# Kernel tuning notes

Hardware: AMD Instinct MI355X
Metric: run time of the kernel (lower is better)

Reference implementation:

```python
import jax, jax.numpy as jnp
import numpy as np

NUM_HEADS = 8


def _layernorm(x, w, b, eps=1e-5):
    # normalize over last axis (channels)
    mu = jnp.mean(x, axis=-1, keepdims=True)
    var = jnp.var(x, axis=-1, keepdims=True)
    return (x - mu) * jax.lax.rsqrt(var + eps) * w + b


def setup_inputs() -> dict:
    key = jax.random.key(0)
    ks = jax.random.split(key, 5)
    B, C, H, W = 8, 512, 32, 32
    x = jax.random.normal(ks[0], (B, C, H, W), dtype=jnp.float32)
    ln_w = jnp.ones((C,), dtype=jnp.float32)
    ln_b = jnp.zeros((C,), dtype=jnp.float32)
    qkv_w = jax.random.normal(ks[1], (3 * C, C), dtype=jnp.float32) * (1.0 / np.sqrt(C))
    qkv_b = jax.random.normal(ks[2], (3 * C,), dtype=jnp.float32) * 0.02
    proj_w = jax.random.normal(ks[3], (C, C), dtype=jnp.float32) * (1.0 / np.sqrt(C))
    proj_b = jax.random.normal(ks[4], (C,), dtype=jnp.float32) * 0.02
    return {"x": x, "ln_w": ln_w, "ln_b": ln_b, "qkv_w": qkv_w,
            "qkv_b": qkv_b, "proj_w": proj_w, "proj_b": proj_b}


def reference(x, ln_w, ln_b, qkv_w, qkv_b, proj_w, proj_b):
    B, C, H, W = x.shape
    nh = NUM_HEADS
    hd = C // nh
    HW = H * W
    residual = x
    # LayerNorm over channels: (B,C,H,W) -> (B,H,W,C)
    xn = _layernorm(x.transpose(0, 2, 3, 1), ln_w, ln_b)  # (B,H,W,C)
    # 1x1 conv == per-pixel linear: (B,H,W,3C)
    qkv = jnp.einsum('bhwc,oc->bhwo', xn, qkv_w) + qkv_b
    # match torch reshape (B,3,nh,hd,HW).permute(1,0,2,4,3)
    qkv = qkv.reshape(B, HW, 3, nh, hd).transpose(2, 0, 3, 1, 4)  # (3,B,nh,HW,hd)
    q, k, v = qkv[0], qkv[1], qkv[2]
    scale = 1.0 / jnp.sqrt(jnp.asarray(hd, dtype=x.dtype))
    attn = jnp.einsum('bnqd,bnkd->bnqk', q, k) * scale  # (B,nh,HW,HW)
    attn = jax.nn.softmax(attn, axis=-1)
    out = jnp.einsum('bnqk,bnkd->bnqd', attn, v)  # (B,nh,HW,hd)
    out = out.transpose(0, 2, 1, 3).reshape(B, H, W, C)
    out = jnp.einsum('bhwc,oc->bhwo', out, proj_w) + proj_b
    return out.transpose(0, 3, 1, 2) + residual
```

## Files before the change

kernel.cpp:

```cpp
#include <hip/hip_runtime.h>

typedef __bf16 bf16;
typedef __bf16 bf16x8 __attribute__((ext_vector_type(8)));
typedef float f32x4 __attribute__((ext_vector_type(4)));
typedef float f32x16 __attribute__((ext_vector_type(16)));

#define MFMA16(a, b, c) __builtin_amdgcn_mfma_f32_16x16x32_bf16(a, b, c, 0, 0, 0)
#define MFMA32(a, b, c) __builtin_amdgcn_mfma_f32_32x32x16_bf16(a, b, c, 0, 0, 0)

#define QSCALE 0.1803368801111137f

static __device__ __forceinline__ unsigned int pack2(float a, float b) {
  unsigned short s0 = __builtin_bit_cast(unsigned short, (bf16)a);
  unsigned short s1 = __builtin_bit_cast(unsigned short, (bf16)b);
  return (unsigned int)s0 | ((unsigned int)s1 << 16);
}

static __device__ __forceinline__ void gl16(const bf16* g, bf16* l) {
  __builtin_amdgcn_global_load_lds(
      (const __attribute__((address_space(1))) unsigned int*)g,
      (__attribute__((address_space(3))) unsigned int*)l, 16, 0, 0);
}

__global__ __launch_bounds__(256) void convert_w(const float* __restrict__ qkvw,
                                                 const float* __restrict__ projw,
                                                 bf16* __restrict__ wc) {
  int c4 = blockIdx.x * 256 + threadIdx.x;
  const float* src = (c4 < 196608) ? (qkvw + (size_t)c4 * 4)
                                   : (projw + (size_t)(c4 - 196608) * 4);
  float4 v = *(const float4*)src;
  uint2 o;
  o.x = pack2(v.x, v.y);
  o.y = pack2(v.z, v.w);
  *(uint2*)&wc[(size_t)c4 * 4] = o;
}

__global__ __launch_bounds__(256) void ln_kernel(const float* __restrict__ x,
                                                 const float* __restrict__ lnw,
                                                 const float* __restrict__ lnb,
                                                 bf16* __restrict__ xn) {
  __shared__ float tile[512 * 17];
  __shared__ float wsh[512];
  __shared__ float bsh[512];
  const int t = threadIdx.x;
  const int b = blockIdx.x >> 6;
  const int p0 = (blockIdx.x & 63) * 16;
  for (int i = t; i < 512; i += 256) {
    wsh[i] = lnw[i];
    bsh[i] = lnb[i];
  }
  const float* xb = x + (size_t)b * 524288 + p0;
#pragma unroll
  for (int i = 0; i < 8; ++i) {
    int chunk = t + 256 * i;
    int c = chunk >> 2, px4 = (chunk & 3) * 4;
    float4 v = *(const float4*)&xb[(size_t)c * 1024 + px4];
    tile[c * 17 + px4 + 0] = v.x;
    tile[c * 17 + px4 + 1] = v.y;
    tile[c * 17 + px4 + 2] = v.z;
    tile[c * 17 + px4 + 3] = v.w;
  }
  __syncthreads();
  const int pix = t >> 4, j = t & 15;
  float sum = 0.f, sq = 0.f;
#pragma unroll
  for (int i = 0; i < 32; ++i) {
    int c = i * 16 + j;
    float v = tile[c * 17 + pix];
    sum += v;
    sq += v * v;
  }
#pragma unroll
  for (int m = 1; m <= 8; m <<= 1) {
    sum += __shfl_xor(sum, m);
    sq += __shfl_xor(sq, m);
  }
  float mu = sum * (1.f / 512.f);
  float var = sq * (1.f / 512.f) - mu * mu;
  float rstd = rsqrtf(var + 1e-5f);
  unsigned int* orow =
      (unsigned int*)(xn + ((size_t)(b * 1024 + p0 + pix)) * 512);
#pragma unroll
  for (int i = 0; i < 16; ++i) {
    int dw = i * 16 + j;
    int c0 = 2 * dw, c1 = 2 * dw + 1;
    float v0 = (tile[c0 * 17 + pix] - mu) * rstd * wsh[c0] + bsh[c0];
    float v1 = (tile[c1 * 17 + pix] - mu) * rstd * wsh[c1] + bsh[c1];
    orow[dw] = pack2(v0, v1);
  }
}

__global__ __launch_bounds__(256, 3) void gemm_qkv(
    const bf16* __restrict__ A, const bf16* __restrict__ Bm,
    const float* __restrict__ bias, bf16* __restrict__ oq,
    bf16* __restrict__ okk, bf16* __restrict__ ov) {
  __shared__ bf16 smem[16384];
  bf16* ash = smem;
  bf16* bsh = smem + 8192;
  const int t = threadIdx.x;
  const int lane = t & 63, w = t >> 6;
  const int quad = lane >> 4, r16 = lane & 15;
  const int wm = w >> 1, wn = w & 1;
  const int pid = blockIdx.x;
  const int panel = pid / 96, within = pid % 96;
  const int m0 = (panel * 8 + (within & 7)) * 128;
  const int n0 = (within >> 3) * 128;
  int soff[4];
  int sr[4];
#pragma unroll
  for (int j = 0; j < 4; ++j) {
    int c = (w * 4 + j) * 64 + lane;
    int r = c >> 3, cc = c & 7;
    sr[j] = r;
    soff[j] = (cc ^ (r & 7)) * 8;
  }
  f32x4 acc[4][4] = {};
  for (int k0 = 0; k0 < 512; k0 += 64) {
#pragma unroll
    for (int j = 0; j < 4; ++j) {
      gl16(&A[(size_t)(m0 + sr[j]) * 512 + k0 + soff[j]],
           &ash[(w * 4 + j) * 512]);
      gl16(&Bm[(size_t)(n0 + sr[j]) * 512 + k0 + soff[j]],
           &bsh[(w * 4 + j) * 512]);
    }
    __syncthreads();
#pragma unroll
    for (int kc = 0; kc < 2; ++kc) {
      bf16x8 af[4], bfr[4];
#pragma unroll
      for (int i = 0; i < 4; ++i) {
        int row = wm * 64 + i * 16 + r16;
        af[i] = *(const bf16x8*)&ash[row * 64 +
                                     ((kc * 4 + quad) ^ (r16 & 7)) * 8];
      }
#pragma unroll
      for (int i = 0; i < 4; ++i) {
        int row = wn * 64 + i * 16 + r16;
        bfr[i] = *(const bf16x8*)&bsh[row * 64 +
                                      ((kc * 4 + quad) ^ (r16 & 7)) * 8];
      }
#pragma unroll
      for (int tm = 0; tm < 4; ++tm)
#pragma unroll
        for (int tn = 0; tn < 4; ++tn)
          acc[tm][tn] = MFMA16(af[tm], bfr[tn], acc[tm][tn]);
    }
    __syncthreads();
  }
  if (n0 < 1024) {
#pragma unroll
    for (int tm = 0; tm < 4; ++tm) {
#pragma unroll
      for (int tn = 0; tn < 4; ++tn) {
        int n = n0 + wn * 64 + tn * 16 + r16;
        float bn = bias[n];
        int comp = n >> 9, h = (n >> 6) & 7, d = n & 63;
#pragma unroll
        for (int r = 0; r < 4; ++r) {
          int m = m0 + wm * 64 + tm * 16 + quad * 4 + r;
          float v = acc[tm][tn][r] + bn;
          int b = m >> 10, p = m & 1023;
          size_t base = ((size_t)(b * 8 + h)) * 65536;
          if (comp == 0)
            oq[base + (size_t)p * 64 + d] = (bf16)(v * QSCALE);
          else
            okk[base + (size_t)p * 64 + d] = (bf16)v;
        }
      }
    }
  } else {
    bf16* tb = &smem[w * 4096];
#pragma unroll
    for (int tn = 0; tn < 4; ++tn) {
      int n = n0 + wn * 64 + tn * 16 + r16;
      float bn = bias[n];
      int row = tn * 16 + r16;
#pragma unroll
      for (int tm = 0; tm < 4; ++tm) {
        f32x4 a = acc[tm][tn];
        uint2 pk;
        pk.x = pack2(a[0] + bn, a[1] + bn);
        pk.y = pack2(a[2] + bn, a[3] + bn);
        int g = (tm * 2 + (quad & 1)) ^ (row & 7);
        *(uint2*)&tb[row * 64 + g * 8 + (quad >> 1) * 4] = pk;
      }
    }
    const int h = ((n0 - 1024) >> 6) + wn;
    const int mw = m0 + wm * 64;
    const int b = mw >> 10;
    bf16* vbase = ov + ((size_t)(b * 8 + h)) * 65536 + (mw & 1023);
#pragma unroll
    for (int pass = 0; pass < 8; ++pass) {
      int row = pass * 8 + (lane >> 3);
      int g = (lane & 7) ^ (row & 7);
      uint4 vd = *(uint4*)&tb[row * 64 + g * 8];
      *(uint4*)&vbase[(size_t)row * 1024 + (lane & 7) * 8] = vd;
    }
  }
}

__global__ __launch_bounds__(256, 4) void gemm_proj(
    const bf16* __restrict__ Wm, const bf16* __restrict__ A,
    const float* __restrict__ bias, const float* __restrict__ resid,
    float* __restrict__ op) {
  __shared__ bf16 ash[2][64 * 64];
  __shared__ bf16 bsh[2][64 * 64];
  const int t = threadIdx.x;
  const int lane = t & 63, w = t >> 6;
  const int quad = lane >> 4, r16 = lane & 15;
  const int wm = w >> 1, wn = w & 1;
  const int m0 = blockIdx.x * 64, n0 = blockIdx.y * 64;
  int soff[2], sr[2];
#pragma unroll
  for (int j = 0; j < 2; ++j) {
    int c = (w * 2 + j) * 64 + lane;
    int r = c >> 3, cc = c & 7;
    sr[j] = r;
    soff[j] = (cc ^ (r & 7)) * 8;
  }
  f32x4 acc[2][2] = {};
#pragma unroll
  for (int j = 0; j < 2; ++j) {
    gl16(&Wm[(size_t)(m0 + sr[j]) * 512 + soff[j]], &ash[0][(w * 2 + j) * 512]);
    gl16(&A[(size_t)(n0 + sr[j]) * 512 + soff[j]], &bsh[0][(w * 2 + j) * 512]);
  }
  __syncthreads();
  for (int it = 0; it < 8; ++it) {
    const int cur = it & 1, nxt = cur ^ 1;
    if (it < 7) {
      int k1 = (it + 1) * 64;
#pragma unroll
      for (int j = 0; j < 2; ++j) {
        gl16(&Wm[(size_t)(m0 + sr[j]) * 512 + k1 + soff[j]],
             &ash[nxt][(w * 2 + j) * 512]);
        gl16(&A[(size_t)(n0 + sr[j]) * 512 + k1 + soff[j]],
             &bsh[nxt][(w * 2 + j) * 512]);
      }
    }
#pragma unroll
    for (int kc = 0; kc < 2; ++kc) {
      bf16x8 af[2], bfr[2];
#pragma unroll
      for (int i = 0; i < 2; ++i) {
        int row = wm * 32 + i * 16 + r16;
        af[i] = *(const bf16x8*)&ash[cur][row * 64 +
                                          ((kc * 4 + quad) ^ (r16 & 7)) * 8];
      }
#pragma unroll
      for (int i = 0; i < 2; ++i) {
        int row = wn * 32 + i * 16 + r16;
        bfr[i] = *(const bf16x8*)&bsh[cur][row * 64 +
                                           ((kc * 4 + quad) ^ (r16 & 7)) * 8];
      }
#pragma unroll
      for (int tm = 0; tm < 2; ++tm)
#pragma unroll
        for (int tn = 0; tn < 2; ++tn)
          acc[tm][tn] = MFMA16(af[tm], bfr[tn], acc[tm][tn]);
    }
    __syncthreads();
  }
#pragma unroll
  for (int tm = 0; tm < 2; ++tm) {
#pragma unroll
    for (int tn = 0; tn < 2; ++tn) {
      int n = n0 + wn * 32 + tn * 16 + r16;
      int b = n >> 10, p = n & 1023;
#pragma unroll
      for (int r = 0; r < 4; ++r) {
        int m = m0 + wm * 32 + tm * 16 + quad * 4 + r;
        size_t idx = ((size_t)(b * 512 + m)) * 1024 + p;
        op[idx] = acc[tm][tn][r] + bias[m] + resid[idx];
      }
    }
  }
}

__global__ __launch_bounds__(256, 2) void attn_kernel(
    const bf16* __restrict__ q, const bf16* __restrict__ k,
    const bf16* __restrict__ vT, bf16* __restrict__ o) {
  __shared__ bf16 kt[2][64 * 64];
  __shared__ bf16 vt[2][64 * 64];
  const int t = threadIdx.x;
  const int lane = t & 63, w = t >> 6;
  const int l31 = lane & 31, hi = lane >> 5;
  const int bh = blockIdx.x;
  const int qt0 = blockIdx.y * 128;
  const bf16* qb = q + (size_t)bh * 65536;
  const bf16* kb = k + (size_t)bh * 65536;
  const bf16* vb = vT + (size_t)bh * 65536;
  const int qrow = qt0 + w * 32 + l31;
  bf16x8 qf[4];
#pragma unroll
  for (int ks = 0; ks < 4; ++ks)
    qf[ks] = *(const bf16x8*)&qb[(size_t)qrow * 64 + ks * 16 + hi * 8];
  int offk[2], offv[2];
#pragma unroll
  for (int j = 0; j < 2; ++j) {
    int c = (w * 2 + j) * 64 + lane;
    int r = c >> 3, cc = c & 7;
    int sw = (cc ^ (r & 7)) * 8;
    offk[j] = r * 64 + sw;
    offv[j] = r * 1024 + sw;
  }
  f32x16 oacc[2] = {};
  float rsum = 0.f;
  const int swz = l31 & 7;
#pragma unroll
  for (int j = 0; j < 2; ++j) {
    gl16(&kb[offk[j]], &kt[0][(w * 2 + j) * 512]);
    gl16(&vb[offv[j]], &vt[0][(w * 2 + j) * 512]);
  }
  __syncthreads();
  for (int it = 0; it < 16; ++it) {
    const int cur = it & 1, nxt = cur ^ 1;
    if (it < 15) {
      int kv1 = (it + 1) * 64;
#pragma unroll
      for (int j = 0; j < 2; ++j) {
        gl16(&kb[(size_t)kv1 * 64 + offk[j]], &kt[nxt][(w * 2 + j) * 512]);
        gl16(&vb[(size_t)kv1 + offv[j]], &vt[nxt][(w * 2 + j) * 512]);
      }
    }
    const bf16* ktc = kt[cur];
    const bf16* vtc = vt[cur];
    f32x16 sT[2] = {};
#pragma unroll
    for (int T = 0; T < 2; ++T) {
      const bf16* kr = &ktc[(T * 32 + l31) * 64];
#pragma unroll
      for (int ks = 0; ks < 4; ++ks) {
        bf16x8 kf = *(const bf16x8*)&kr[((ks * 2 + hi) ^ swz) * 8];
        sT[T] = MFMA32(kf, qf[ks], sT[T]);
      }
    }
#pragma unroll
    for (int T = 0; T < 2; ++T)
#pragma unroll
      for (int r = 0; r < 16; ++r) {
        float p = __builtin_exp2f(sT[T][r]);
        sT[T][r] = p;
        rsum += p;
      }
#pragma unroll
    for (int c4 = 0; c4 < 4; ++c4) {
      const int T = c4 >> 1, b0 = (c4 & 1) * 8;
      uint4 pui;
      pui.x = pack2(sT[T][b0 + 0], sT[T][b0 + 1]);
      pui.y = pack2(sT[T][b0 + 2], sT[T][b0 + 3]);
      pui.z = pack2(sT[T][b0 + 4], sT[T][b0 + 5]);
      pui.w = pack2(sT[T][b0 + 6], sT[T][b0 + 7]);
      bf16x8 pf = __builtin_bit_cast(bf16x8, pui);
#pragma unroll
      for (int mf = 0; mf < 2; ++mf) {
        const bf16* vr = &vtc[(mf * 32 + l31) * 64];
        bf16x8 vf = *(const bf16x8*)&vr[((c4 * 2 + hi) ^ swz) * 8];
        oacc[mf] = MFMA32(pf, vf, oacc[mf]);
      }
    }
    __syncthreads();
  }
  rsum += __shfl_xor(rsum, 32);
  float inv = 1.f / rsum;
  const int b = bh >> 3, h = bh & 7;
#pragma unroll
  for (int r = 0; r < 16; ++r) {
    const int ql = (r & 3) + 8 * (r >> 2) + 4 * hi;
    float invq = __shfl(inv, ql);
    const int p = qt0 + w * 32 + ql;
    const size_t base = ((size_t)(b * 1024 + p)) * 512 + h * 64;
#pragma unroll
    for (int mf = 0; mf < 2; ++mf)
      o[base + mf * 32 + l31] = (bf16)(oacc[mf][r] * invq);
  }
}

extern "C" void kernel_launch(void* const* d_in, const int* in_sizes, int n_in,
                              void* d_out, int out_size, void* d_ws,
                              size_t ws_size, hipStream_t stream) {
  (void)in_sizes;
  (void)n_in;
  (void)out_size;
  (void)ws_size;
  const float* x = (const float*)d_in[0];
  const float* lnw = (const float*)d_in[1];
  const float* lnb = (const float*)d_in[2];
  const float* qkvw = (const float*)d_in[3];
  const float* qkvb = (const float*)d_in[4];
  const float* projw = (const float*)d_in[5];
  const float* projb = (const float*)d_in[6];
  float* out = (float*)d_out;

  const size_t NELEM = 4194304;
  bf16* wc = (bf16*)d_ws;
  bf16* xn = wc + 1048576;
  bf16* qws = xn + NELEM;
  bf16* kws = qws + NELEM;
  bf16* vws = kws + NELEM;
  bf16* aws = xn;

  convert_w<<<dim3(1024), dim3(256), 0, stream>>>(qkvw, projw, wc);
  ln_kernel<<<dim3(512), dim3(256), 0, stream>>>(x, lnw, lnb, xn);
  gemm_qkv<<<dim3(768), dim3(256), 0, stream>>>(xn, wc, qkvb, qws, kws, vws);
  attn_kernel<<<dim3(64, 8), dim3(256), 0, stream>>>(qws, kws, vws, aws);
  gemm_proj<<<dim3(8, 128), dim3(256), 0, stream>>>(wc + 786432, aws, projb, x,
                                                    out);
}
```

Baseline: 153.3 us.

## Merge weight conversion and layernorm launches; double-buffer QKV GEMM K-loop

Fuses the weight-to-bf16 conversion and layernorm kernels into one launch, with blocks split by index, to save a kernel launch. Restructures the QKV GEMM from single-buffered 64-wide K tiles to double-buffered 32-wide K tiles, so the next tile's global-to-LDS loads overlap the current MFMAs. The new LDS layout drops the XOR swizzle, which may bring bank conflicts on the fragment reads. The fused kernel also reserves the large LDS tile for the conversion blocks, which may reduce their occupancy.

```diff
diff --git a/kernel.cpp b/kernel.cpp
--- a/kernel.cpp
+++ b/kernel.cpp
@@ -22,29 +22,29 @@
       (__attribute__((address_space(3))) unsigned int*)l, 16, 0, 0);
 }
 
-__global__ __launch_bounds__(256) void convert_w(const float* __restrict__ qkvw,
-                                                 const float* __restrict__ projw,
-                                                 bf16* __restrict__ wc) {
-  int c4 = blockIdx.x * 256 + threadIdx.x;
-  const float* src = (c4 < 196608) ? (qkvw + (size_t)c4 * 4)
-                                   : (projw + (size_t)(c4 - 196608) * 4);
-  float4 v = *(const float4*)src;
-  uint2 o;
-  o.x = pack2(v.x, v.y);
-  o.y = pack2(v.z, v.w);
-  *(uint2*)&wc[(size_t)c4 * 4] = o;
-}
-
-__global__ __launch_bounds__(256) void ln_kernel(const float* __restrict__ x,
-                                                 const float* __restrict__ lnw,
-                                                 const float* __restrict__ lnb,
-                                                 bf16* __restrict__ xn) {
+__global__ __launch_bounds__(256) void prep_kernel(
+    const float* __restrict__ qkvw, const float* __restrict__ projw,
+    bf16* __restrict__ wc, const float* __restrict__ x,
+    const float* __restrict__ lnw, const float* __restrict__ lnb,
+    bf16* __restrict__ xn) {
   __shared__ float tile[512 * 17];
   __shared__ float wsh[512];
   __shared__ float bsh[512];
   const int t = threadIdx.x;
-  const int b = blockIdx.x >> 6;
-  const int p0 = (blockIdx.x & 63) * 16;
+  if (blockIdx.x < 1024) {
+    int c4 = blockIdx.x * 256 + t;
+    const float* src = (c4 < 196608) ? (qkvw + (size_t)c4 * 4)
+                                     : (projw + (size_t)(c4 - 196608) * 4);
+    float4 v = *(const float4*)src;
+    uint2 o;
+    o.x = pack2(v.x, v.y);
+    o.y = pack2(v.z, v.w);
+    *(uint2*)&wc[(size_t)c4 * 4] = o;
+    return;
+  }
+  const int bid = blockIdx.x - 1024;
+  const int b = bid >> 6;
+  const int p0 = (bid & 63) * 16;
   for (int i = t; i < 512; i += 256) {
     wsh[i] = lnw[i];
     bsh[i] = lnb[i];
@@ -95,8 +95,6 @@
     const float* __restrict__ bias, bf16* __restrict__ oq,
     bf16* __restrict__ okk, bf16* __restrict__ ov) {
   __shared__ bf16 smem[16384];
-  bf16* ash = smem;
-  bf16* bsh = smem + 8192;
   const int t = threadIdx.x;
   const int lane = t & 63, w = t >> 6;
   const int quad = lane >> 4, r16 = lane & 15;
@@ -105,46 +103,51 @@
   const int panel = pid / 96, within = pid % 96;
   const int m0 = (panel * 8 + (within & 7)) * 128;
   const int n0 = (within >> 3) * 128;
-  int soff[4];
-  int sr[4];
-#pragma unroll
-  for (int j = 0; j < 4; ++j) {
-    int c = (w * 4 + j) * 64 + lane;
-    int r = c >> 3, cc = c & 7;
-    sr[j] = r;
-    soff[j] = (cc ^ (r & 7)) * 8;
+  int sr[2], sc[2];
+#pragma unroll
+  for (int j = 0; j < 2; ++j) {
+    int c = (w * 2 + j) * 64 + lane;
+    sr[j] = c >> 2;
+    sc[j] = (c & 3) * 8;
   }
   f32x4 acc[4][4] = {};
-  for (int k0 = 0; k0 < 512; k0 += 64) {
-#pragma unroll
-    for (int j = 0; j < 4; ++j) {
-      gl16(&A[(size_t)(m0 + sr[j]) * 512 + k0 + soff[j]],
-           &ash[(w * 4 + j) * 512]);
-      gl16(&Bm[(size_t)(n0 + sr[j]) * 512 + k0 + soff[j]],
-           &bsh[(w * 4 + j) * 512]);
-    }
-    __syncthreads();
-#pragma unroll
-    for (int kc = 0; kc < 2; ++kc) {
-      bf16x8 af[4], bfr[4];
-#pragma unroll
-      for (int i = 0; i < 4; ++i) {
-        int row = wm * 64 + i * 16 + r16;
-        af[i] = *(const bf16x8*)&ash[row * 64 +
-                                     ((kc * 4 + quad) ^ (r16 & 7)) * 8];
-      }
-#pragma unroll
-      for (int i = 0; i < 4; ++i) {
-        int row = wn * 64 + i * 16 + r16;
-        bfr[i] = *(const bf16x8*)&bsh[row * 64 +
-                                      ((kc * 4 + quad) ^ (r16 & 7)) * 8];
-      }
-#pragma unroll
-      for (int tm = 0; tm < 4; ++tm)
-#pragma unroll
-        for (int tn = 0; tn < 4; ++tn)
-          acc[tm][tn] = MFMA16(af[tm], bfr[tn], acc[tm][tn]);
-    }
+#pragma unroll
+  for (int j = 0; j < 2; ++j) {
+    gl16(&A[(size_t)(m0 + sr[j]) * 512 + sc[j]], &smem[(w * 2 + j) * 512]);
+    gl16(&Bm[(size_t)(n0 + sr[j]) * 512 + sc[j]],
+         &smem[8192 + (w * 2 + j) * 512]);
+  }
+  __syncthreads();
+  for (int it = 0; it < 16; ++it) {
+    const int cur = it & 1, nxt = cur ^ 1;
+    if (it < 15) {
+      int k1 = (it + 1) * 32;
+#pragma unroll
+      for (int j = 0; j < 2; ++j) {
+        gl16(&A[(size_t)(m0 + sr[j]) * 512 + k1 + sc[j]],
+             &smem[nxt * 4096 + (w * 2 + j) * 512]);
+        gl16(&Bm[(size_t)(n0 + sr[j]) * 512 + k1 + sc[j]],
+             &smem[8192 + nxt * 4096 + (w * 2 + j) * 512]);
+      }
+    }
+    const bf16* ac = &smem[cur * 4096];
+    const bf16* bc = &smem[8192 + cur * 4096];
+    bf16x8 af[4], bfr[4];
+#pragma unroll
+    for (int i = 0; i < 4; ++i) {
+      int row = wm * 64 + i * 16 + r16;
+      af[i] = *(const bf16x8*)&ac[row * 32 + quad * 8];
+    }
+#pragma unroll
+    for (int i = 0; i < 4; ++i) {
+      int row = wn * 64 + i * 16 + r16;
+      bfr[i] = *(const bf16x8*)&bc[row * 32 + quad * 8];
+    }
+#pragma unroll
+    for (int tm = 0; tm < 4; ++tm)
+#pragma unroll
+      for (int tn = 0; tn < 4; ++tn)
+        acc[tm][tn] = MFMA16(af[tm], bfr[tn], acc[tm][tn]);
     __syncthreads();
   }
   if (n0 < 1024) {
@@ -399,8 +402,8 @@
   bf16* vws = kws + NELEM;
   bf16* aws = xn;
 
-  convert_w<<<dim3(1024), dim3(256), 0, stream>>>(qkvw, projw, wc);
-  ln_kernel<<<dim3(512), dim3(256), 0, stream>>>(x, lnw, lnb, xn);
+  prep_kernel<<<dim3(1536), dim3(256), 0, stream>>>(qkvw, projw, wc, x, lnw,
+                                                    lnb, xn);
   gemm_qkv<<<dim3(768), dim3(256), 0, stream>>>(xn, wc, qkvb, qws, kws, vws);
   attn_kernel<<<dim3(64, 8), dim3(256), 0, stream>>>(qws, kws, vws, aws);
   gemm_proj<<<dim3(8, 128), dim3(256), 0, stream>>>(wc + 786432, aws, projb, x,
```

After: 152.0 us. No clear change (-0.8%).
